# Optimization experiments

Hardware: AMD Instinct MI355X
Metric: run time of the kernel (lower is better)

Reference implementation:

```python
import jax, jax.numpy as jnp
import numpy as np

H, N2, R = 512, 16, 32   # hidden_dim, state_dim//2, dt_rank=ceil(512/16)
B, L = 1, 4096


def setup_inputs() -> dict:
    key = jax.random.key(0)
    ks = jax.random.split(key, 7)
    u = jax.random.normal(ks[0], (B, L, H), dtype=jnp.float32)
    # Parameter initialization mirroring S4DKernel.__init__
    A_log = jnp.zeros((H, N2), jnp.float32)                      # log(ones)
    A_im = jnp.broadcast_to(jnp.arange(N2, dtype=jnp.float32), (H, N2)).copy()
    B_param = jax.random.normal(ks[1], (H, N2, 2), jnp.float32)
    C_param = jax.random.normal(ks[2], (H, N2, 2), jnp.float32)
    D = jax.random.normal(ks[3], (H,), jnp.float32)
    dt_w = jax.random.normal(ks[4], (H, R), jnp.float32) / np.sqrt(R)
    dt_min, dt_max, dt_floor = 1e-3, 0.1, 1e-4
    dt_init = jnp.exp(jax.random.uniform(ks[5], (H,), jnp.float32)
                      * (np.log(dt_max) - np.log(dt_floor)) + np.log(dt_floor))
    dt_init = jnp.maximum(dt_init, dt_min)
    dt_b = dt_init + jnp.log(-jnp.expm1(-dt_init))               # inverse-softplus init
    xproj_w = jax.random.normal(ks[6], (R, H), jnp.float32) / np.sqrt(H)
    return {"u": u, "A_log": A_log, "A_im": A_im, "B_param": B_param,
            "C_param": C_param, "D": D, "dt_w": dt_w, "dt_b": dt_b,
            "xproj_w": xproj_w}


def reference(u, A_log, A_im, B_param, C_param, D, dt_w, dt_b, xproj_w):
    # Complex continuous-time parameters
    A = -jnp.exp(A_log) + 1j * A_im                 # [H, N2]
    Bc = B_param[..., 0] + 1j * B_param[..., 1]     # [H, N2]
    Cc = C_param[..., 0] + 1j * C_param[..., 1]     # [H, N2]

    # dt path: x_proj_for_dt (no bias) -> dt_proj -> softplus
    dt_u = jnp.einsum('blh,rh->blr', u, xproj_w)                    # [B,L,R]
    dt = jax.nn.softplus(jnp.einsum('blr,hr->blh', dt_u, dt_w) + dt_b)  # [B,L,H]

    # ZOH discretization
    z = dt[..., None] * A                           # [B,L,H,N2] complex
    A_bar = jnp.exp(z)
    B_bar_div = jnp.where(jnp.abs(z) < 1e-4, 1.0 + z / 2, (jnp.exp(z) - 1.0) / z)
    ub = u[..., None].astype(A_bar.dtype) * B_bar_div * Bc          # [B,L,H,N2]

    # Parallel scan for h_k = A_k * h_{k-1} + u_k (first-order linear recurrence)
    def op(c1, c2):
        a1, b1 = c1
        a2, b2 = c2
        return a1 * a2, a2 * b1 + b2
    _, h = jax.lax.associative_scan(op, (A_bar, ub), axis=1)        # [B,L,H,N2]

    y = jnp.einsum('blhn,hn->blh', h, Cc) + u * D
    return y.real
```

## Files before the change

kernel.cpp:

```cpp
#include <hip/hip_runtime.h>

#define Hd 512
#define N2d 16
#define Rd 32
#define Ld 4096
#define NCHUNK 256
#define CLEN (Ld / NCHUNK)
#define NCH (Hd * N2d)
#define NGRP 16
#define NGROUPS (NCHUNK / NGRP)

__global__ __launch_bounds__(256) void k_tw(const float* __restrict__ dt_w,
                                            float* __restrict__ dt_wT) {
    int idx = blockIdx.x * 256 + threadIdx.x;
    int r = idx >> 9;
    int h = idx & 511;
    dt_wT[idx] = dt_w[h * Rd + r];
}

__device__ __forceinline__ bool load_consts4(const float* A_log, const float* A_im,
        const float* B_param, int hnb,
        float* Are, float* Aim, float* BAr, float* BAi) {
    #pragma unroll
    for (int j = 0; j < 4; ++j) {
        int hn = hnb + j;
        Are[j] = -__expf(A_log[hn]);
        Aim[j] = A_im[hn];
        float Bre = B_param[2 * hn];
        float Bim = B_param[2 * hn + 1];
        float inv = __builtin_amdgcn_rcpf(Are[j] * Are[j] + Aim[j] * Aim[j]);
        BAr[j] = (Bre * Are[j] + Bim * Aim[j]) * inv;
        BAi[j] = (Bim * Are[j] - Bre * Aim[j]) * inv;
    }
    float d1 = Aim[1] - Aim[0], d2 = Aim[2] - Aim[1], d3 = Aim[3] - Aim[2];
    return (Are[1] == Are[0]) && (Are[2] == Are[0]) && (Are[3] == Are[0]) &&
           (d1 == d2) && (d2 == d3);
}

__global__ __launch_bounds__(256) void k_dt(const float* __restrict__ u,
                                            const float* __restrict__ xproj_w,
                                            const float* __restrict__ dt_wT,
                                            const float* __restrict__ dt_b,
                                            float2* __restrict__ du_out) {
    __shared__ float u_s[8][Hd];
    __shared__ float dtu_s[8][Rd];
    const int t = threadIdx.x;
    const int l0 = blockIdx.x * 8;

    #pragma unroll
    for (int i = 0; i < 16; ++i) {
        int idx = t + i * 256;
        ((float*)u_s)[idx] = u[l0 * Hd + idx];
    }
    __syncthreads();

    const int r = t >> 3;
    const int j = t & 7;
    float part[8];
    #pragma unroll
    for (int l = 0; l < 8; ++l) part[l] = 0.f;
    for (int k = 0; k < 64; ++k) {
        float w = xproj_w[r * Hd + k * 8 + j];
        #pragma unroll
        for (int l = 0; l < 8; ++l) part[l] = fmaf(u_s[l][k * 8 + j], w, part[l]);
    }
    #pragma unroll
    for (int off = 1; off < 8; off <<= 1) {
        #pragma unroll
        for (int l = 0; l < 8; ++l) part[l] += __shfl_xor(part[l], off);
    }
    if (j == 0) {
        #pragma unroll
        for (int l = 0; l < 8; ++l) dtu_s[l][r] = part[l];
    }
    __syncthreads();

    #pragma unroll
    for (int hb = 0; hb < 2; ++hb) {
        int h = hb * 256 + t;
        float bias = dt_b[h];
        float acc[8];
        #pragma unroll
        for (int l = 0; l < 8; ++l) acc[l] = bias;
        for (int rr = 0; rr < Rd; ++rr) {
            float w = dt_wT[rr * Hd + h];
            #pragma unroll
            for (int l = 0; l < 8; ++l) acc[l] = fmaf(dtu_s[l][rr], w, acc[l]);
        }
        #pragma unroll
        for (int l = 0; l < 8; ++l) {
            float x = acc[l];
            float sp = fmaxf(x, 0.f) + log1pf(__expf(-fabsf(x)));
            float uv = u_s[l][h];
            float us = uv * __builtin_amdgcn_rcpf(fmaxf(sp, 1e-30f));
            du_out[(l0 + l) * Hd + h] = make_float2(sp, us);
        }
    }
}

__global__ __launch_bounds__(256) void k_chunk(const float2* __restrict__ du,
        const float* __restrict__ A_log, const float* __restrict__ A_im,
        const float* __restrict__ B_param,
        float2* __restrict__ Pbuf, float2* __restrict__ Sbuf) {
    const int t = threadIdx.x;
    const int q = t & 3;
    const int hh = blockIdx.y * 64 + (t >> 2);
    const int c = blockIdx.x;
    const int hnb = hh * N2d + q * 4;
    const int lbase = c * CLEN;

    float2 d[CLEN];
    #pragma unroll
    for (int k = 0; k < CLEN; ++k) d[k] = du[(lbase + k) * Hd + hh];

    float Are[4], Aim[4], BAr[4], BAi[4];
    const bool fast = load_consts4(A_log, A_im, B_param, hnb, Are, Aim, BAr, BAi);
    float sr[4] = {0.f, 0.f, 0.f, 0.f}, si[4] = {0.f, 0.f, 0.f, 0.f};
    float sdt = 0.f;
    if (fast) {
        const float Are0 = Are[0], Aim0 = Aim[0], dA = Aim[1] - Aim[0];
        #pragma unroll
        for (int k = 0; k < CLEN; ++k) {
            float dtv = d[k].x, us = d[k].y;
            sdt += dtv;
            float er = __expf(dtv * Are0);
            float s0, c0, sd, cd;
            __sincosf(dtv * Aim0, &s0, &c0);
            __sincosf(dtv * dA, &sd, &cd);
            float ar = er * c0, ai = er * s0;
            #pragma unroll
            for (int jj = 0; jj < 4; ++jj) {
                float gr = fmaf(ar, us, -us);
                float gi = ai * us;
                float nr = fmaf(ar, sr[jj], fmaf(-ai, si[jj], fmaf(gr, BAr[jj], -gi * BAi[jj])));
                float ni = fmaf(ar, si[jj], fmaf( ai, sr[jj], fmaf(gr, BAi[jj],  gi * BAr[jj])));
                sr[jj] = nr; si[jj] = ni;
                if (jj < 3) {
                    float tr = fmaf(ar, cd, -ai * sd);
                    ai = fmaf(ai, cd, ar * sd);
                    ar = tr;
                }
            }
        }
    } else {
        #pragma unroll
        for (int k = 0; k < CLEN; ++k) {
            float dtv = d[k].x, us = d[k].y;
            sdt += dtv;
            #pragma unroll
            for (int jj = 0; jj < 4; ++jj) {
                float er = __expf(dtv * Are[jj]);
                float s, cc;
                __sincosf(dtv * Aim[jj], &s, &cc);
                float ar = er * cc, ai = er * s;
                float gr = fmaf(ar, us, -us);
                float gi = ai * us;
                float nr = fmaf(ar, sr[jj], fmaf(-ai, si[jj], fmaf(gr, BAr[jj], -gi * BAi[jj])));
                float ni = fmaf(ar, si[jj], fmaf( ai, sr[jj], fmaf(gr, BAi[jj],  gi * BAr[jj])));
                sr[jj] = nr; si[jj] = ni;
            }
        }
    }
    int base = c * NCH + hnb;
    #pragma unroll
    for (int jj = 0; jj < 4; ++jj) {
        float er = __expf(sdt * Are[jj]);
        float s, cc;
        __sincosf(sdt * Aim[jj], &s, &cc);
        Pbuf[base + jj] = make_float2(er * cc, er * s);
        Sbuf[base + jj] = make_float2(sr[jj], si[jj]);
    }
}

__global__ __launch_bounds__(256) void k_group(const float2* __restrict__ Pbuf,
        const float2* __restrict__ Sbuf, float2* __restrict__ Ilocal,
        float2* __restrict__ Pcum, float2* __restrict__ Gp,
        float2* __restrict__ Gs) {
    int idx = blockIdx.x * 256 + threadIdx.x;
    int chain = idx & (NCH - 1);
    int g = idx >> 13;
    float pr = 1.f, pi = 0.f, hr = 0.f, hi = 0.f;
    #pragma unroll
    for (int half = 0; half < 2; ++half) {
        float2 tp[8], ts[8];
        #pragma unroll
        for (int i = 0; i < 8; ++i) {
            int c = g * NGRP + half * 8 + i;
            tp[i] = Pbuf[c * NCH + chain];
            ts[i] = Sbuf[c * NCH + chain];
        }
        #pragma unroll
        for (int i = 0; i < 8; ++i) {
            int c = g * NGRP + half * 8 + i;
            Ilocal[c * NCH + chain] = make_float2(hr, hi);
            Pcum[c * NCH + chain]   = make_float2(pr, pi);
            float nhr = fmaf(tp[i].x, hr, fmaf(-tp[i].y, hi, ts[i].x));
            float nhi = fmaf(tp[i].x, hi, fmaf( tp[i].y, hr, ts[i].y));
            float npr = fmaf(tp[i].x, pr, -tp[i].y * pi);
            float npi = fmaf(tp[i].x, pi,  tp[i].y * pr);
            hr = nhr; hi = nhi; pr = npr; pi = npi;
        }
    }
    Gp[g * NCH + chain] = make_float2(pr, pi);
    Gs[g * NCH + chain] = make_float2(hr, hi);
}

__global__ __launch_bounds__(256) void k_gscan(const float2* __restrict__ Gp,
        const float2* __restrict__ Gs, float2* __restrict__ H0g) {
    int chain = blockIdx.x * 256 + threadIdx.x;
    float2 gp[NGROUPS], gs[NGROUPS];
    #pragma unroll
    for (int g = 0; g < NGROUPS; ++g) {
        gp[g] = Gp[g * NCH + chain];
        gs[g] = Gs[g * NCH + chain];
    }
    float hr = 0.f, hi = 0.f;
    #pragma unroll
    for (int g = 0; g < NGROUPS; ++g) {
        H0g[g * NCH + chain] = make_float2(hr, hi);
        float nr = fmaf(gp[g].x, hr, fmaf(-gp[g].y, hi, gs[g].x));
        float ni = fmaf(gp[g].x, hi, fmaf( gp[g].y, hr, gs[g].y));
        hr = nr; hi = ni;
    }
}

__global__ __launch_bounds__(256) void k_scan(const float2* __restrict__ du,
        const float* __restrict__ A_log, const float* __restrict__ A_im,
        const float* __restrict__ B_param, const float* __restrict__ C_param,
        const float* __restrict__ Dp, const float2* __restrict__ Ilocal,
        const float2* __restrict__ Pcum, const float2* __restrict__ H0g,
        float* __restrict__ out) {
    const int t = threadIdx.x;
    const int q = t & 3;
    const int hh = blockIdx.y * 64 + (t >> 2);
    const int c = blockIdx.x;
    const int g = c / NGRP;
    const int hnb = hh * N2d + q * 4;
    const int lbase = c * CLEN;

    float2 d[CLEN];
    #pragma unroll
    for (int k = 0; k < CLEN; ++k) d[k] = du[(lbase + k) * Hd + hh];

    float Are[4], Aim[4], BAr[4], BAi[4], Cre[4], Cim[4];
    const bool fast = load_consts4(A_log, A_im, B_param, hnb, Are, Aim, BAr, BAi);
    #pragma unroll
    for (int jj = 0; jj < 4; ++jj) {
        Cre[jj] = C_param[2 * (hnb + jj)];
        Cim[jj] = C_param[2 * (hnb + jj) + 1];
    }
    const float Dv = Dp[hh];
    float hr[4], hi[4];
    #pragma unroll
    for (int jj = 0; jj < 4; ++jj) {
        int ch = c * NCH + hnb + jj;
        float2 il = Ilocal[ch];
        float2 pc = Pcum[ch];
        float2 hg = H0g[g * NCH + hnb + jj];
        hr[jj] = fmaf(pc.x, hg.x, fmaf(-pc.y, hg.y, il.x));
        hi[jj] = fmaf(pc.x, hg.y, fmaf( pc.y, hg.x, il.y));
    }

    if (fast) {
        const float Are0 = Are[0], Aim0 = Aim[0], dA = Aim[1] - Aim[0];
        #pragma unroll
        for (int k = 0; k < CLEN; ++k) {
            int l = lbase + k;
            float dtv = d[k].x, us = d[k].y;
            float er = __expf(dtv * Are0);
            float s0, c0, sd, cd;
            __sincosf(dtv * Aim0, &s0, &c0);
            __sincosf(dtv * dA, &sd, &cd);
            float ar = er * c0, ai = er * s0;
            float yv = 0.f;
            #pragma unroll
            for (int jj = 0; jj < 4; ++jj) {
                float gr = fmaf(ar, us, -us);
                float gi = ai * us;
                float nr = fmaf(ar, hr[jj], fmaf(-ai, hi[jj], fmaf(gr, BAr[jj], -gi * BAi[jj])));
                float ni = fmaf(ar, hi[jj], fmaf( ai, hr[jj], fmaf(gr, BAi[jj],  gi * BAr[jj])));
                hr[jj] = nr; hi[jj] = ni;
                yv = fmaf(nr, Cre[jj], fmaf(-ni, Cim[jj], yv));
                if (jj < 3) {
                    float tr = fmaf(ar, cd, -ai * sd);
                    ai = fmaf(ai, cd, ar * sd);
                    ar = tr;
                }
            }
            yv += __shfl_xor(yv, 1);
            yv += __shfl_xor(yv, 2);
            if (q == 0) out[l * Hd + hh] = fmaf(dtv * us, Dv, yv);
        }
    } else {
        #pragma unroll
        for (int k = 0; k < CLEN; ++k) {
            int l = lbase + k;
            float dtv = d[k].x, us = d[k].y;
            float yv = 0.f;
            #pragma unroll
            for (int jj = 0; jj < 4; ++jj) {
                float er = __expf(dtv * Aim[jj] * 0.f + dtv * Are[jj]);
                float s, cc;
                __sincosf(dtv * Aim[jj], &s, &cc);
                float ar = er * cc, ai = er * s;
                float gr = fmaf(ar, us, -us);
                float gi = ai * us;
                float nr = fmaf(ar, hr[jj], fmaf(-ai, hi[jj], fmaf(gr, BAr[jj], -gi * BAi[jj])));
                float ni = fmaf(ar, hi[jj], fmaf( ai, hr[jj], fmaf(gr, BAi[jj],  gi * BAr[jj])));
                hr[jj] = nr; hi[jj] = ni;
                yv = fmaf(nr, Cre[jj], fmaf(-ni, Cim[jj], yv));
            }
            yv += __shfl_xor(yv, 1);
            yv += __shfl_xor(yv, 2);
            if (q == 0) out[l * Hd + hh] = fmaf(dtv * us, Dv, yv);
        }
    }
}

extern "C" void kernel_launch(void* const* d_in, const int* in_sizes, int n_in,
                              void* d_out, int out_size, void* d_ws, size_t ws_size,
                              hipStream_t stream) {
    const float* u        = (const float*)d_in[0];
    const float* A_log    = (const float*)d_in[1];
    const float* A_im     = (const float*)d_in[2];
    const float* B_param  = (const float*)d_in[3];
    const float* C_param  = (const float*)d_in[4];
    const float* Dp       = (const float*)d_in[5];
    const float* dt_w     = (const float*)d_in[6];
    const float* dt_b     = (const float*)d_in[7];
    const float* xproj_w  = (const float*)d_in[8];

    float2* du     = (float2*)d_ws;
    float2* Pbuf   = du + (size_t)Ld * Hd;
    float2* Sbuf   = Pbuf + (size_t)NCHUNK * NCH;
    float2* Ilocal = Sbuf + (size_t)NCHUNK * NCH;
    float2* Pcum   = Ilocal + (size_t)NCHUNK * NCH;
    float2* Gp     = Pcum + (size_t)NCHUNK * NCH;
    float2* Gs     = Gp + (size_t)NGROUPS * NCH;
    float2* H0g    = Gs + (size_t)NGROUPS * NCH;
    float*  dt_wT  = (float*)(H0g + (size_t)NGROUPS * NCH);
    float*  out    = (float*)d_out;

    k_tw<<<(Rd * Hd) / 256, 256, 0, stream>>>(dt_w, dt_wT);
    k_dt<<<Ld / 8, 256, 0, stream>>>(u, xproj_w, dt_wT, dt_b, du);
    dim3 g2(NCHUNK, Hd / 64);
    k_chunk<<<g2, 256, 0, stream>>>(du, A_log, A_im, B_param, Pbuf, Sbuf);
    k_group<<<(NCH * NGROUPS) / 256, 256, 0, stream>>>(Pbuf, Sbuf, Ilocal, Pcum, Gp, Gs);
    k_gscan<<<NCH / 256, 256, 0, stream>>>(Gp, Gs, H0g);
    k_scan<<<g2, 256, 0, stream>>>(du, A_log, A_im, B_param, C_param, Dp,
                                   Ilocal, Pcum, H0g, out);
}
```

Before: 149.7 us.

## Restructure chunk-scan prefix: pack P/S, drop Ilocal/Pcum, recompute in-group prefix

Interleaves chunk decay and state into one float4 buffer and replaces the group kernel with a reduce-only aggregation, so the per-chunk Ilocal/Pcum arrays are no longer written or read. The final scan kernel instead walks the preceding chunks in its group (up to 7, with the group size halved to 8) starting from the group prefix. The dt_w transpose kernel is removed and k_dt reads dt_w rows directly as float4. This saves one launch and a lot of intermediate global traffic, at the cost of redundant serial prefix work in k_scan and uncoalesced per-thread row reads of dt_w.

Measured after the change: 163.3 us. +9.0%, slower.

```diff
diff --git a/kernel.cpp b/kernel.cpp
--- a/kernel.cpp
+++ b/kernel.cpp
@@ -7,16 +7,8 @@
 #define NCHUNK 256
 #define CLEN (Ld / NCHUNK)
 #define NCH (Hd * N2d)
-#define NGRP 16
+#define NGRP 8
 #define NGROUPS (NCHUNK / NGRP)
-
-__global__ __launch_bounds__(256) void k_tw(const float* __restrict__ dt_w,
-                                            float* __restrict__ dt_wT) {
-    int idx = blockIdx.x * 256 + threadIdx.x;
-    int r = idx >> 9;
-    int h = idx & 511;
-    dt_wT[idx] = dt_w[h * Rd + r];
-}
 
 __device__ __forceinline__ bool load_consts4(const float* A_log, const float* A_im,
         const float* B_param, int hnb,
@@ -39,7 +31,7 @@
 
 __global__ __launch_bounds__(256) void k_dt(const float* __restrict__ u,
                                             const float* __restrict__ xproj_w,
-                                            const float* __restrict__ dt_wT,
+                                            const float* __restrict__ dt_w,
                                             const float* __restrict__ dt_b,
                                             float2* __restrict__ du_out) {
     __shared__ float u_s[8][Hd];
@@ -82,10 +74,16 @@
         float acc[8];
         #pragma unroll
         for (int l = 0; l < 8; ++l) acc[l] = bias;
-        for (int rr = 0; rr < Rd; ++rr) {
-            float w = dt_wT[rr * Hd + h];
-            #pragma unroll
-            for (int l = 0; l < 8; ++l) acc[l] = fmaf(dtu_s[l][rr], w, acc[l]);
+        #pragma unroll
+        for (int rb = 0; rb < 8; ++rb) {
+            float4 w = *(const float4*)&dt_w[h * Rd + rb * 4];
+            #pragma unroll
+            for (int l = 0; l < 8; ++l) {
+                acc[l] = fmaf(dtu_s[l][rb * 4 + 0], w.x, acc[l]);
+                acc[l] = fmaf(dtu_s[l][rb * 4 + 1], w.y, acc[l]);
+                acc[l] = fmaf(dtu_s[l][rb * 4 + 2], w.z, acc[l]);
+                acc[l] = fmaf(dtu_s[l][rb * 4 + 3], w.w, acc[l]);
+            }
         }
         #pragma unroll
         for (int l = 0; l < 8; ++l) {
@@ -100,8 +98,7 @@
 
 __global__ __launch_bounds__(256) void k_chunk(const float2* __restrict__ du,
         const float* __restrict__ A_log, const float* __restrict__ A_im,
-        const float* __restrict__ B_param,
-        float2* __restrict__ Pbuf, float2* __restrict__ Sbuf) {
+        const float* __restrict__ B_param, float4* __restrict__ PS) {
     const int t = threadIdx.x;
     const int q = t & 3;
     const int hh = blockIdx.y * 64 + (t >> 2);
@@ -167,74 +164,61 @@
         float er = __expf(sdt * Are[jj]);
         float s, cc;
         __sincosf(sdt * Aim[jj], &s, &cc);
-        Pbuf[base + jj] = make_float2(er * cc, er * s);
-        Sbuf[base + jj] = make_float2(sr[jj], si[jj]);
-    }
-}
-
-__global__ __launch_bounds__(256) void k_group(const float2* __restrict__ Pbuf,
-        const float2* __restrict__ Sbuf, float2* __restrict__ Ilocal,
-        float2* __restrict__ Pcum, float2* __restrict__ Gp,
-        float2* __restrict__ Gs) {
+        PS[base + jj] = make_float4(er * cc, er * s, sr[jj], si[jj]);
+    }
+}
+
+__global__ __launch_bounds__(256) void k_gagg(const float4* __restrict__ PS,
+                                              float4* __restrict__ Gps) {
     int idx = blockIdx.x * 256 + threadIdx.x;
     int chain = idx & (NCH - 1);
     int g = idx >> 13;
+    float4 ps[NGRP];
+    #pragma unroll
+    for (int i = 0; i < NGRP; ++i)
+        ps[i] = PS[(g * NGRP + i) * NCH + chain];
     float pr = 1.f, pi = 0.f, hr = 0.f, hi = 0.f;
     #pragma unroll
-    for (int half = 0; half < 2; ++half) {
-        float2 tp[8], ts[8];
+    for (int i = 0; i < NGRP; ++i) {
+        float nhr = fmaf(ps[i].x, hr, fmaf(-ps[i].y, hi, ps[i].z));
+        float nhi = fmaf(ps[i].x, hi, fmaf( ps[i].y, hr, ps[i].w));
+        float npr = fmaf(ps[i].x, pr, -ps[i].y * pi);
+        float npi = fmaf(ps[i].x, pi,  ps[i].y * pr);
+        hr = nhr; hi = nhi; pr = npr; pi = npi;
+    }
+    Gps[g * NCH + chain] = make_float4(pr, pi, hr, hi);
+}
+
+__global__ __launch_bounds__(256) void k_gscan(const float4* __restrict__ Gps,
+                                               float2* __restrict__ H0g) {
+    int chain = blockIdx.x * 256 + threadIdx.x;
+    float hr = 0.f, hi = 0.f;
+    #pragma unroll
+    for (int gb = 0; gb < NGROUPS / 8; ++gb) {
+        float4 gp[8];
+        #pragma unroll
+        for (int i = 0; i < 8; ++i)
+            gp[i] = Gps[(gb * 8 + i) * NCH + chain];
         #pragma unroll
         for (int i = 0; i < 8; ++i) {
-            int c = g * NGRP + half * 8 + i;
-            tp[i] = Pbuf[c * NCH + chain];
-            ts[i] = Sbuf[c * NCH + chain];
-        }
-        #pragma unroll
-        for (int i = 0; i < 8; ++i) {
-            int c = g * NGRP + half * 8 + i;
-            Ilocal[c * NCH + chain] = make_float2(hr, hi);
-            Pcum[c * NCH + chain]   = make_float2(pr, pi);
-            float nhr = fmaf(tp[i].x, hr, fmaf(-tp[i].y, hi, ts[i].x));
-            float nhi = fmaf(tp[i].x, hi, fmaf( tp[i].y, hr, ts[i].y));
-            float npr = fmaf(tp[i].x, pr, -tp[i].y * pi);
-            float npi = fmaf(tp[i].x, pi,  tp[i].y * pr);
-            hr = nhr; hi = nhi; pr = npr; pi = npi;
-        }
-    }
-    Gp[g * NCH + chain] = make_float2(pr, pi);
-    Gs[g * NCH + chain] = make_float2(hr, hi);
-}
-
-__global__ __launch_bounds__(256) void k_gscan(const float2* __restrict__ Gp,
-        const float2* __restrict__ Gs, float2* __restrict__ H0g) {
-    int chain = blockIdx.x * 256 + threadIdx.x;
-    float2 gp[NGROUPS], gs[NGROUPS];
-    #pragma unroll
-    for (int g = 0; g < NGROUPS; ++g) {
-        gp[g] = Gp[g * NCH + chain];
-        gs[g] = Gs[g * NCH + chain];
-    }
-    float hr = 0.f, hi = 0.f;
-    #pragma unroll
-    for (int g = 0; g < NGROUPS; ++g) {
-        H0g[g * NCH + chain] = make_float2(hr, hi);
-        float nr = fmaf(gp[g].x, hr, fmaf(-gp[g].y, hi, gs[g].x));
-        float ni = fmaf(gp[g].x, hi, fmaf( gp[g].y, hr, gs[g].y));
-        hr = nr; hi = ni;
+            H0g[(gb * 8 + i) * NCH + chain] = make_float2(hr, hi);
+            float nr = fmaf(gp[i].x, hr, fmaf(-gp[i].y, hi, gp[i].z));
+            float ni = fmaf(gp[i].x, hi, fmaf( gp[i].y, hr, gp[i].w));
+            hr = nr; hi = ni;
+        }
     }
 }
 
 __global__ __launch_bounds__(256) void k_scan(const float2* __restrict__ du,
         const float* __restrict__ A_log, const float* __restrict__ A_im,
         const float* __restrict__ B_param, const float* __restrict__ C_param,
-        const float* __restrict__ Dp, const float2* __restrict__ Ilocal,
-        const float2* __restrict__ Pcum, const float2* __restrict__ H0g,
-        float* __restrict__ out) {
+        const float* __restrict__ Dp, const float4* __restrict__ PS,
+        const float2* __restrict__ H0g, float* __restrict__ out) {
     const int t = threadIdx.x;
     const int q = t & 3;
     const int hh = blockIdx.y * 64 + (t >> 2);
     const int c = blockIdx.x;
-    const int g = c / NGRP;
+    const int g = c >> 3;
     const int hnb = hh * N2d + q * 4;
     const int lbase = c * CLEN;
 
@@ -250,15 +234,23 @@
         Cim[jj] = C_param[2 * (hnb + jj) + 1];
     }
     const float Dv = Dp[hh];
+
     float hr[4], hi[4];
     #pragma unroll
     for (int jj = 0; jj < 4; ++jj) {
-        int ch = c * NCH + hnb + jj;
-        float2 il = Ilocal[ch];
-        float2 pc = Pcum[ch];
-        float2 hg = H0g[g * NCH + hnb + jj];
-        hr[jj] = fmaf(pc.x, hg.x, fmaf(-pc.y, hg.y, il.x));
-        hi[jj] = fmaf(pc.x, hg.y, fmaf( pc.y, hg.x, il.y));
+        float2 h0 = H0g[g * NCH + hnb + jj];
+        hr[jj] = h0.x; hi[jj] = h0.y;
+    }
+    for (int cp = g * NGRP; cp < c; ++cp) {
+        float4 ps[4];
+        #pragma unroll
+        for (int jj = 0; jj < 4; ++jj) ps[jj] = PS[cp * NCH + hnb + jj];
+        #pragma unroll
+        for (int jj = 0; jj < 4; ++jj) {
+            float nr = fmaf(ps[jj].x, hr[jj], fmaf(-ps[jj].y, hi[jj], ps[jj].z));
+            float ni = fmaf(ps[jj].x, hi[jj], fmaf( ps[jj].y, hr[jj], ps[jj].w));
+            hr[jj] = nr; hi[jj] = ni;
+        }
     }
 
     if (fast) {
@@ -299,7 +291,7 @@
             float yv = 0.f;
             #pragma unroll
             for (int jj = 0; jj < 4; ++jj) {
-                float er = __expf(dtv * Aim[jj] * 0.f + dtv * Are[jj]);
+                float er = __expf(dtv * Are[jj]);
                 float s, cc;
                 __sincosf(dtv * Aim[jj], &s, &cc);
                 float ar = er * cc, ai = er * s;
@@ -330,23 +322,17 @@
     const float* dt_b     = (const float*)d_in[7];
     const float* xproj_w  = (const float*)d_in[8];
 
-    float2* du     = (float2*)d_ws;
-    float2* Pbuf   = du + (size_t)Ld * Hd;
-    float2* Sbuf   = Pbuf + (size_t)NCHUNK * NCH;
-    float2* Ilocal = Sbuf + (size_t)NCHUNK * NCH;
-    float2* Pcum   = Ilocal + (size_t)NCHUNK * NCH;
-    float2* Gp     = Pcum + (size_t)NCHUNK * NCH;
-    float2* Gs     = Gp + (size_t)NGROUPS * NCH;
-    float2* H0g    = Gs + (size_t)NGROUPS * NCH;
-    float*  dt_wT  = (float*)(H0g + (size_t)NGROUPS * NCH);
-    float*  out    = (float*)d_out;
-
-    k_tw<<<(Rd * Hd) / 256, 256, 0, stream>>>(dt_w, dt_wT);
-    k_dt<<<Ld / 8, 256, 0, stream>>>(u, xproj_w, dt_wT, dt_b, du);
+    float2* du  = (float2*)d_ws;
+    float4* PS  = (float4*)(du + (size_t)Ld * Hd);
+    float4* Gps = PS + (size_t)NCHUNK * NCH;
+    float2* H0g = (float2*)(Gps + (size_t)NGROUPS * NCH);
+    float*  out = (float*)d_out;
+
+    k_dt<<<Ld / 8, 256, 0, stream>>>(u, xproj_w, dt_w, dt_b, du);
     dim3 g2(NCHUNK, Hd / 64);
-    k_chunk<<<g2, 256, 0, stream>>>(du, A_log, A_im, B_param, Pbuf, Sbuf);
-    k_group<<<(NCH * NGROUPS) / 256, 256, 0, stream>>>(Pbuf, Sbuf, Ilocal, Pcum, Gp, Gs);
-    k_gscan<<<NCH / 256, 256, 0, stream>>>(Gp, Gs, H0g);
+    k_chunk<<<g2, 256, 0, stream>>>(du, A_log, A_im, B_param, PS);
+    k_gagg<<<(NCH * NGROUPS) / 256, 256, 0, stream>>>(PS, Gps);
+    k_gscan<<<NCH / 256, 256, 0, stream>>>(Gps, H0g);
     k_scan<<<g2, 256, 0, stream>>>(du, A_log, A_im, B_param, C_param, Dp,
-                                   Ilocal, Pcum, H0g, out);
-}
+                                   PS, H0g, out);
+}
```
